# Optimization experiments

Measured on AMD Instinct MI355X. Metric: run time of the kernel, lower is better.

Reference implementation:

```python
import jax, jax.numpy as jnp
import numpy as np

B, K, V_DIM, EMBED, HID, NTOKEN, MAX_LEN = 128, 36, 2048, 1024, 1024, 10000, 20


def _u(key, shape, scale=0.05):
    return jax.random.uniform(key, shape, jnp.float32, -scale, scale)


def setup_inputs() -> dict:
    key = jax.random.key(0)
    ks = jax.random.split(key, 12)
    d1 = HID + V_DIM + EMBED  # word_rnn input size
    d2 = V_DIM + HID          # language_rnn input size
    return dict(
        v=jax.random.normal(ks[0], (B, K, V_DIM), jnp.float32),
        caption=jax.random.normal(ks[1], (B, MAX_LEN, EMBED), jnp.float32),
        cap_len=jnp.sort(jax.random.randint(ks[2], (B,), 2, MAX_LEN + 1))[::-1].astype(jnp.int32),
        Wih1=_u(ks[3], (3 * HID, d1)), Whh1=_u(ks[4], (3 * HID, HID)),
        bih1=jnp.zeros((3 * HID,), jnp.float32), bhh1=jnp.zeros((3 * HID,), jnp.float32),
        Wih2=_u(ks[5], (3 * HID, d2)), Whh2=_u(ks[6], (3 * HID, HID)),
        bih2=jnp.zeros((3 * HID,), jnp.float32), bhh2=jnp.zeros((3 * HID,), jnp.float32),
        Wv=_u(ks[7], (HID, V_DIM)), bv=jnp.zeros((HID,), jnp.float32),
        Wq=_u(ks[8], (HID, HID)), bq=jnp.zeros((HID,), jnp.float32),
        wa=_u(ks[9], (HID,)), ba=jnp.zeros((), jnp.float32),
        W1=_u(ks[10], (HID, HID)), b1=jnp.zeros((HID,), jnp.float32),
        W2=_u(ks[11], (NTOKEN, HID)), b2=jnp.zeros((NTOKEN,), jnp.float32),
    )


def _gru(x, h, Wih, Whh, bih, bhh):
    # PyTorch GRUCell math, gate order (r, z, n)
    gi = x @ Wih.T + bih
    gh = h @ Whh.T + bhh
    ir, iz, inn = jnp.split(gi, 3, axis=-1)
    hr, hz, hn = jnp.split(gh, 3, axis=-1)
    r = jax.nn.sigmoid(ir + hr)
    z = jax.nn.sigmoid(iz + hz)
    n = jnp.tanh(inn + r * hn)
    return (1.0 - z) * n + z * h


def reference(v, caption, cap_len, Wih1, Whh1, bih1, bhh1, Wih2, Whh2, bih2, bhh2,
              Wv, bv, Wq, bq, wa, ba, W1, b1, W2, b2):
    # sort by caption length, descending (as torch forward does)
    order = jnp.argsort(-cap_len)
    v = v[order]
    caption = caption[order]
    cap_len = cap_len[order]
    v_mean = v.mean(1)                                  # [B, V_DIM]
    vproj = jax.nn.relu(v @ Wv.T + bv)                  # [B, K, HID], hoisted out of time loop

    T = MAX_LEN - 1
    dl = cap_len - 1                                    # decode lengths
    mask = (jnp.arange(T)[:, None] < dl[None, :]).astype(v.dtype)   # [T, B]
    prevs = jnp.swapaxes(caption[:, :T, :], 0, 1)       # [T, B, EMBED]

    def step(carry, xs):
        h1, h2 = carry
        prev, m = xs
        h1n = _gru(jnp.concatenate([h2, v_mean, prev], axis=1), h1, Wih1, Whh1, bih1, bhh1)
        hq = h1n @ W1.T + b1                            # h1_fcnet (dropout = identity in eval)
        # 'base' attention: softmax over objects of w^T(relu(Wv v) * relu(Wq q))
        logits = (vproj * jax.nn.relu(hq @ Wq.T + bq)[:, None, :]) @ wa + ba   # [B, K]
        att = jax.nn.softmax(logits, axis=1)
        att_v = jnp.einsum('bk,bkd->bd', att, v)        # attended image feature
        h2n = _gru(jnp.concatenate([att_v, hq], axis=1), h2, Wih2, Whh2, bih2, bhh2)
        word = h2n @ W2.T + b2                          # [B, NTOKEN]
        return (h1n, h2n), (word * m[:, None], att * m[:, None])

    init = (jnp.zeros((B, HID), v.dtype), jnp.zeros((B, HID), v.dtype))
    _, (words, atts) = jax.lax.scan(step, init, (prevs, mask))
    # pad back to max_len timesteps as the torch output buffer does
    predict = jnp.pad(jnp.swapaxes(words, 0, 1), ((0, 0), (0, 1), (0, 0)))   # [B, MAX_LEN, NTOKEN]
    alphas = jnp.pad(jnp.swapaxes(atts, 0, 1), ((0, 0), (0, 1), (0, 0)))     # [B, MAX_LEN, K]
    return predict, alphas
```

## Files before the change

### kernel.cpp

```cpp
#include <hip/hip_runtime.h>
#include <hip/hip_cooperative_groups.h>

namespace cg = cooperative_groups;

typedef unsigned short u16;
typedef __attribute__((ext_vector_type(8))) short bf16x8;
typedef __attribute__((ext_vector_type(4))) float f32x4;

#define NB 128
#define NOBJ 36
#define VDIM 2048
#define EMB 1024
#define HID 1024
#define NTOK 10000
#define MAXLEN 20
#define T_STEPS 19
#define PRED_STRIDE (MAXLEN * NTOK)
#define ALPHA_OFF ((long)NB * MAXLEN * NTOK)
#define HSZ (NB * HID)

struct Args {
  const float *v, *caption;
  const int *cap_len;
  const float *Wih1, *Whh1, *bih1, *bhh1, *Wih2, *Whh2, *bih2, *bhh2;
  const float *Wv, *bv, *Wq, *bq, *wa, *ba, *W1, *b1, *W2, *b2;
  float *out;
  int *order, *dl;
  u16 *Wih1h, *Whh1h, *Wih2h, *Whh2h, *Wvh, *W2h, *vh, *caph, *capl;
  u16 *Wqh, *Wql, *W1T, *Wih2hql, *Wq1u, *Wih2qu;
  u16 *vproj16;
  float *gv1, *gh2s, *h1f, *h2f, *qf, *gcap, *g1a, *g1c, *g2a, *g2b, *gi2h1;
  float *bq1f, *bf2f;
  u16 *h1hi, *h1lo, *h2hi, *h2lo, *avhi, *avlo, *vmhi, *vmlo;
};

__device__ inline float b2f(u16 h) {
  unsigned u = ((unsigned)h) << 16;
  float f;
  __builtin_memcpy(&f, &u, 4);
  return f;
}
__device__ inline u16 f2b_trunc(float x) {
  unsigned u;
  __builtin_memcpy(&u, &x, 4);
  return (u16)(u >> 16);
}
__device__ inline u16 f2b_rne(float x) {
  unsigned u;
  __builtin_memcpy(&u, &x, 4);
  unsigned r = (u + 0x7fffu + ((u >> 16) & 1u)) >> 16;
  return (u16)r;
}
__device__ inline void split_bf16(float x, u16 &hi, u16 &lo) {
  hi = f2b_trunc(x);
  lo = f2b_trunc(x - b2f(hi));
}
__device__ inline bf16x8 ldb8(const u16 *p) {
  uint4 u = *(const uint4 *)p;
  bf16x8 v;
  __builtin_memcpy(&v, &u, 16);
  return v;
}
__device__ inline f32x4 mfma16(bf16x8 a, bf16x8 b, f32x4 c) {
  return __builtin_amdgcn_mfma_f32_16x16x32_bf16(a, b, c, 0, 0, 0);
}
__device__ inline float sigmoidf_(float x) {
  float e = __expf(-fabsf(x));
  float p = 1.f / (1.f + e);
  return x >= 0.f ? p : 1.f - p;
}
__device__ inline float tanhf_(float x) {
  float e = __expf(-2.f * fabsf(x));
  float t = (1.f - e) / (1.f + e);
  return x >= 0.f ? t : -t;
}
__device__ inline float wred_sum(float x) {
#pragma unroll
  for (int off = 32; off > 0; off >>= 1) x += __shfl_xor(x, off, 64);
  return x;
}
__device__ inline float wred_max(float x) {
#pragma unroll
  for (int off = 32; off > 0; off >>= 1) x = fmaxf(x, __shfl_xor(x, off, 64));
  return x;
}

__device__ inline void cvt_hi(const float *src, u16 *dst, long n, long g0,
                              long gs) {
  for (long i = g0 * 4; i < n; i += gs * 4) {
    float4 f = *(const float4 *)(src + i);
    ushort4 o;
    o.x = f2b_rne(f.x);
    o.y = f2b_rne(f.y);
    o.z = f2b_rne(f.z);
    o.w = f2b_rne(f.w);
    *(ushort4 *)(dst + i) = o;
  }
}
__device__ inline void cvt_split(const float *src, u16 *dhi, u16 *dlo, long n,
                                 long g0, long gs) {
  for (long i = g0 * 4; i < n; i += gs * 4) {
    float4 f = *(const float4 *)(src + i);
    ushort4 h, l;
    split_bf16(f.x, h.x, l.x);
    split_bf16(f.y, h.y, l.y);
    split_bf16(f.z, h.z, l.z);
    split_bf16(f.w, h.w, l.w);
    *(ushort4 *)(dhi + i) = h;
    *(ushort4 *)(dlo + i) = l;
  }
}

#define MMK_BODY                                                               \
  {                                                                            \
    const int ko = ks * 32;                                                    \
    bf16x8 va = ldb8(ah + ko);                                                 \
    bf16x8 vl;                                                                 \
    if constexpr (SPLIT) vl = ldb8(al + ko);                                   \
    _Pragma("unroll") for (int i = 0; i < NT; ++i) {                           \
      bf16x8 vb = ldb8(wr + (long)i * wstride + ko);                           \
      acc[i] = mfma16(va, vb, acc[i]);                                         \
      if constexpr (SPLIT) acc[i] = mfma16(vl, vb, acc[i]);                    \
    }                                                                          \
  }

template <int NT, bool SPLIT>
__device__ inline void mmk(f32x4 *acc, const u16 *ah, const u16 *al,
                           const u16 *wr, long wstride, int ksteps) {
  if constexpr (NT == 1) {
#pragma unroll 4
    for (int ks = 0; ks < ksteps; ++ks) MMK_BODY
  } else {
#pragma unroll 2
    for (int ks = 0; ks < ksteps; ++ks) MMK_BODY
  }
}

template <bool SPLIT>
__device__ inline f32x4 tile16(const u16 *ah, const u16 *al, const u16 *wr,
                               int K) {
  f32x4 acc = {0.f, 0.f, 0.f, 0.f};
  mmk<1, SPLIT>(&acc, ah, al, wr, 0, K >> 5);
  return acc;
}

__global__ void __launch_bounds__(512, 4) butd(Args a) {
  cg::grid_group grid = cg::this_grid();
  const int tid = threadIdx.x;
  const int blk = blockIdx.x;
  const int gx = gridDim.x;
  const int lane = tid & 63;
  const int wv = tid >> 6;
  const int m = lane & 15;
  const int quad = lane >> 4;
  __shared__ float sl[64];

  const long gs = (long)gx * 512;
  const long g0 = (long)blk * 512 + tid;

  cvt_hi(a.Wih1, a.Wih1h, 3072L * 4096, g0, gs);
  cvt_hi(a.Whh1, a.Whh1h, 3072L * 1024, g0, gs);
  cvt_hi(a.Wih2, a.Wih2h, 3072L * 3072, g0, gs);
  cvt_hi(a.Whh2, a.Whh2h, 3072L * 1024, g0, gs);
  cvt_hi(a.Wv, a.Wvh, 1024L * 2048, g0, gs);
  cvt_hi(a.W2, a.W2h, (long)NTOK * 1024, g0, gs);
  cvt_hi(a.v, a.vh, (long)NB * NOBJ * VDIM, g0, gs);
  cvt_split(a.caption, a.caph, a.capl, (long)NB * MAXLEN * EMB, g0, gs);
  cvt_split(a.Wq, a.Wqh, a.Wql, 1024L * 1024, g0, gs);
  for (long i = g0; i < 1024L * 1024; i += gs) {
    const int ii = (int)(i >> 10), mm2 = (int)(i & 1023);
    a.W1T[i] = f2b_rne(a.W1[(long)mm2 * 1024 + ii]);
  }
  for (long i = g0 * 4; i < 3072L * 1024; i += gs * 4) {
    const int row = (int)(i >> 10), c = (int)(i & 1023);
    float4 f = *(const float4 *)(a.Wih2 + (long)row * 3072 + 2048 + c);
    ushort4 l;
    l.x = f2b_trunc(f.x - b2f(f2b_rne(f.x)));
    l.y = f2b_trunc(f.y - b2f(f2b_rne(f.y)));
    l.z = f2b_trunc(f.z - b2f(f2b_rne(f.z)));
    l.w = f2b_trunc(f.w - b2f(f2b_rne(f.w)));
    *(ushort4 *)(a.Wih2hql + i) = l;
  }

  if (blk == 0 && tid < NB) {
    int ki = a.cap_len[tid];
    int rank = 0;
    for (int j = 0; j < NB; ++j) {
      int kj = a.cap_len[j];
      rank += (kj > ki) || (kj == ki && j < tid);
    }
    a.order[rank] = tid;
    a.dl[rank] = ki - 1;
  }
  for (long i = g0; i < (long)NB * NTOK; i += gs) {
    long b = i / NTOK, n = i - b * NTOK;
    a.out[b * PRED_STRIDE + (long)(MAXLEN - 1) * NTOK + n] = 0.f;
  }
  for (long i = g0; i < (long)NB * NOBJ; i += gs) {
    long b = i / NOBJ, n = i - b * NOBJ;
    a.out[ALPHA_OFF + b * (MAXLEN * NOBJ) + (MAXLEN - 1) * NOBJ + n] = 0.f;
  }
  for (long i = g0; i < HSZ; i += gs) {
    a.h1f[i] = 0.f;
    a.h2f[i] = 0.f;
    a.h1hi[i] = 0;
    a.h1lo[i] = 0;
    a.h2hi[i] = 0;
    a.h2lo[i] = 0;
  }
  for (long i = g0; i < 128L * 3072; i += gs) a.g1c[i] = 0.f;
  grid.sync();

  for (int b = blk; b < NB; b += gx) {
    const int ob = a.order[b];
    const float *vb = a.v + (long)ob * NOBJ * VDIM;
    for (int d = tid; d < VDIM; d += 512) {
      float s = 0.f;
      for (int k = 0; k < NOBJ; ++k) s += vb[(long)k * VDIM + d];
      s *= (1.f / 36.f);
      u16 hi, lo;
      split_bf16(s, hi, lo);
      a.vmhi[b * VDIM + d] = hi;
      a.vmlo[b * VDIM + d] = lo;
    }
  }
  for (int tt = blk; tt < 576; tt += gx) {
    const int mg = tt % 36, ngr = tt / 36;
    const int row = mg * 128 + wv * 16 + m;
    const int bb = row / NOBJ, ko = row - bb * NOBJ;
    const u16 *ar = a.vh + ((long)a.order[bb] * NOBJ + ko) * VDIM + quad * 8;
    const int c0 = ngr * 64;
    const u16 *wr = a.Wvh + (long)(c0 + m) * VDIM + quad * 8;
    f32x4 acc[4] = {};
    mmk<4, false>(acc, ar, nullptr, wr, 16L * VDIM, VDIM / 32);
#pragma unroll
    for (int i = 0; i < 4; ++i) {
      const int col = c0 + i * 16 + m;
      const float bvv = a.bv[col];
#pragma unroll
      for (int r = 0; r < 4; ++r) {
        const int grow = mg * 128 + wv * 16 + quad * 4 + r;
        a.vproj16[(long)grow * HID + col] = f2b_rne(fmaxf(acc[i][r] + bvv, 0.f));
      }
    }
  }
  for (int o = blk * 8 + wv; o < 4096; o += gx * 8) {
    if (o < 1024) {
      float s = 0.f;
      for (int c = lane; c < 1024; c += 64) s += a.Wq[(long)o * 1024 + c] * a.b1[c];
      s = wred_sum(s);
      if (lane == 0) a.bq1f[o] = s + a.bq[o];
    } else {
      const int oo = o - 1024;
      float s = 0.f;
      for (int c = lane; c < 1024; c += 64)
        s += a.Wih2[(long)oo * 3072 + 2048 + c] * a.b1[c];
      s = wred_sum(s);
      if (lane == 0) a.bf2f[oo] = s;
    }
  }
  grid.sync();

  {
    const int arow = wv * 16 + m;
    for (int task = blk; task < 5888; task += gx) {
      if (task < 192) {
        const int col = task * 16 + m;
        f32x4 acc = tile16<true>(
            a.vmhi + (long)arow * VDIM + quad * 8,
            a.vmlo + (long)arow * VDIM + quad * 8,
            a.Wih1h + (long)col * 4096 + 1024 + quad * 8, VDIM);
        const float bb = a.bih1[col];
#pragma unroll
        for (int r = 0; r < 4; ++r)
          a.gv1[(long)(wv * 16 + quad * 4 + r) * 3072 + col] = acc[r] + bb;
      } else if (task < 3840) {
        const int tt2 = task - 192;
        const int tdx = tt2 / 192, ct = tt2 % 192;
        const int col = ct * 16 + m;
        const long capoff = ((long)a.order[arow] * MAXLEN + tdx) * EMB;
        f32x4 acc = tile16<true>(
            a.caph + capoff + quad * 8, a.capl + capoff + quad * 8,
            a.Wih1h + (long)col * 4096 + 3072 + quad * 8, EMB);
#pragma unroll
        for (int r = 0; r < 4; ++r)
          a.gcap[((long)tdx * NB + wv * 16 + quad * 4 + r) * 3072 + col] =
              acc[r];
      } else if (task < 4352) {
        const int tt2 = task - 3840;
        const int rg = tt2 >> 6, ct = tt2 & 63;
        const int row = rg * 128 + arow, col = ct * 16 + m;
        f32x4 acc = tile16<true>(a.Wqh + (long)row * HID + quad * 8,
                                 a.Wql + (long)row * HID + quad * 8,
                                 a.W1T + (long)col * HID + quad * 8, HID);
#pragma unroll
        for (int r = 0; r < 4; ++r) {
          const int o = rg * 128 + wv * 16 + quad * 4 + r;
          a.Wq1u[(long)o * HID + col] = f2b_rne(acc[r]);
        }
      } else {
        const int tt2 = task - 4352;
        const int rg = tt2 >> 6, ct = tt2 & 63;
        const int row = rg * 128 + arow, col = ct * 16 + m;
        f32x4 acc = tile16<true>(
            a.Wih2h + (long)row * 3072 + 2048 + quad * 8,
            a.Wih2hql + (long)row * HID + quad * 8,
            a.W1T + (long)col * HID + quad * 8, HID);
#pragma unroll
        for (int r = 0; r < 4; ++r) {
          const int o = rg * 128 + wv * 16 + quad * 4 + r;
          a.Wih2qu[(long)o * HID + col] = f2b_rne(acc[r]);
        }
      }
    }
  }
  grid.sync();

  const int arow = wv * 16 + m;

  auto word_tile = [&](int wt, int tf, int pb) {
    const int col = wt * 16 + m;
    f32x4 acc = tile16<true>(
        a.h2hi + (long)pb * HSZ + (long)arow * HID + quad * 8,
        a.h2lo + (long)pb * HSZ + (long)arow * HID + quad * 8,
        a.W2h + (long)col * HID + quad * 8, HID);
    const float bb = a.b2[col];
#pragma unroll
    for (int r = 0; r < 4; ++r) {
      const int grow = wv * 16 + quad * 4 + r;
      const int msk = tf < a.dl[grow];
      a.out[(long)grow * PRED_STRIDE + (long)tf * NTOK + col] =
          msk ? acc[r] + bb : 0.f;
    }
  };

  auto attention = [&](int t, int b, int half) {
    __syncthreads();
    const int ob = a.order[b];
    const float *qrow = a.qf + (long)b * HID;
    for (int k = wv; k < NOBJ; k += 8) {
      const u16 *vp = a.vproj16 + ((long)b * NOBJ + k) * HID;
      float s = 0.f;
      for (int d = lane; d < HID; d += 64) s += b2f(vp[d]) * qrow[d] * a.wa[d];
      s = wred_sum(s);
      if (lane == 0) sl[k] = s + a.ba[0];
    }
    __syncthreads();
    if (wv == 0) {
      float x = (lane < NOBJ) ? sl[lane] : -3.0e38f;
      float mx = wred_max(x);
      float e = (lane < NOBJ) ? __expf(x - mx) : 0.f;
      float den = wred_sum(e);
      float att = e / den;
      if (lane < NOBJ) {
        sl[lane] = att;
        if (half == 0) {
          const int msk = t < a.dl[b];
          a.out[ALPHA_OFF + (long)b * (MAXLEN * NOBJ) + t * NOBJ + lane] =
              msk ? att : 0.f;
        }
      }
    }
    __syncthreads();
    const u16 *vb = a.vh + (long)ob * NOBJ * VDIM + half * 1024;
    for (int d = tid; d < 1024; d += 512) {
      float s = 0.f;
#pragma unroll
      for (int k = 0; k < NOBJ; ++k) s += sl[k] * b2f(vb[(long)k * VDIM + d]);
      u16 hi, lo;
      split_bf16(s, hi, lo);
      a.avhi[(long)b * VDIM + half * 1024 + d] = hi;
      a.avlo[(long)b * VDIM + half * 1024 + d] = lo;
    }
  };

  auto S1 = [&](int t) {
    const int pr = t & 1;
    const u16 *h2h = a.h2hi + (long)pr * HSZ + (long)arow * HID + quad * 8;
    const u16 *h2l = a.h2lo + (long)pr * HSZ + (long)arow * HID + quad * 8;
    for (int task = blk; task < 512; task += gx) {
      if (task < 192) {
        const int col = task * 16 + m;
        f32x4 acc = tile16<true>(h2h, h2l,
                                 a.Wih1h + (long)col * 4096 + quad * 8, HID);
#pragma unroll
        for (int r = 0; r < 4; ++r)
          a.g1a[(long)(wv * 16 + quad * 4 + r) * 3072 + col] = acc[r];
      } else if (task < 384) {
        const int col = (task - 192) * 16 + m;
        f32x4 acc =
            tile16<true>(h2h, h2l, a.Whh2h + (long)col * HID + quad * 8, HID);
        const float bb = a.bhh2[col];
#pragma unroll
        for (int r = 0; r < 4; ++r)
          a.gh2s[(long)(wv * 16 + quad * 4 + r) * 3072 + col] = acc[r] + bb;
      } else if (t > 0) {
        word_tile(task - 384, t - 1, pr);
      }
    }
  };

  auto S2 = [&](int t) {
    const int pr = t & 1, pw_ = pr ^ 1;
    for (long i = g0; i < (long)HSZ; i += gs) {
      const int row = (int)(i >> 10), col = (int)(i & 1023);
      const long o3 = (long)row * 3072 + col;
      const float *gc = a.gcap + ((long)t * NB + row) * 3072 + col;
      float ir = a.g1a[o3] + gc[0] + a.gv1[o3];
      float iz = a.g1a[o3 + 1024] + gc[1024] + a.gv1[o3 + 1024];
      float in_ = a.g1a[o3 + 2048] + gc[2048] + a.gv1[o3 + 2048];
      float hr = a.g1c[o3] + a.bhh1[col];
      float hz = a.g1c[o3 + 1024] + a.bhh1[HID + col];
      float hn = a.g1c[o3 + 2048] + a.bhh1[2 * HID + col];
      float rr = sigmoidf_(ir + hr);
      float zz = sigmoidf_(iz + hz);
      float nn = tanhf_(in_ + rr * hn);
      const long io = (long)pr * HSZ + i, iw = (long)pw_ * HSZ + i;
      float hnew = (1.f - zz) * nn + zz * a.h1f[io];
      a.h1f[iw] = hnew;
      u16 hi, lo;
      split_bf16(hnew, hi, lo);
      a.h1hi[iw] = hi;
      a.h1lo[iw] = lo;
    }
    if (t > 0)
      for (int task = blk; task < 256; task += gx)
        word_tile(128 + task, t - 1, t & 1);
  };

  auto S3 = [&](int t) {
    const int pw_ = (t & 1) ^ 1;
    const u16 *h1h = a.h1hi + (long)pw_ * HSZ + (long)arow * HID + quad * 8;
    const u16 *h1l = a.h1lo + (long)pw_ * HSZ + (long)arow * HID + quad * 8;
    for (int task = blk; task < 497; task += gx) {
      if (task < 64) {
        const int col = task * 16 + m;
        f32x4 acc =
            tile16<true>(h1h, h1l, a.Wq1u + (long)col * HID + quad * 8, HID);
        const float bb = a.bq1f[col];
#pragma unroll
        for (int r = 0; r < 4; ++r)
          a.qf[(long)(wv * 16 + quad * 4 + r) * HID + col] =
              fmaxf(acc[r] + bb, 0.f);
      } else if (task < 256) {
        const int col = (task - 64) * 16 + m;
        f32x4 acc =
            tile16<true>(h1h, h1l, a.Wih2qu + (long)col * HID + quad * 8, HID);
#pragma unroll
        for (int r = 0; r < 4; ++r)
          a.gi2h1[(long)(wv * 16 + quad * 4 + r) * 3072 + col] = acc[r];
      } else if (t > 0) {
        word_tile(384 + (task - 256), t - 1, t & 1);
      }
    }
  };

  auto S4 = [&](int t) {
    const int pw_ = (t & 1) ^ 1;
    for (int task = blk; task < 448; task += gx) {
      if (task < 256) {
        attention(t, task & 127, task >> 7);
      } else if (t + 1 < T_STEPS) {
        const int col = (task - 256) * 16 + m;
        f32x4 acc = tile16<true>(
            a.h1hi + (long)pw_ * HSZ + (long)arow * HID + quad * 8,
            a.h1lo + (long)pw_ * HSZ + (long)arow * HID + quad * 8,
            a.Whh1h + (long)col * HID + quad * 8, HID);
#pragma unroll
        for (int r = 0; r < 4; ++r)
          a.g1c[(long)(wv * 16 + quad * 4 + r) * 3072 + col] = acc[r];
      }
    }
  };

  auto S5 = [&](int t) {
    (void)t;
    for (int task = blk; task < 384; task += gx) {
      const int kh = task / 192, ct = task % 192;
      const int col = ct * 16 + m;
      f32x4 acc = tile16<true>(
          a.avhi + kh * 1024 + (long)arow * VDIM + quad * 8,
          a.avlo + kh * 1024 + (long)arow * VDIM + quad * 8,
          a.Wih2h + (long)col * 3072 + kh * 1024 + quad * 8, HID);
      float *dst = kh ? a.g2b : a.g2a;
#pragma unroll
      for (int r = 0; r < 4; ++r)
        dst[(long)(wv * 16 + quad * 4 + r) * 3072 + col] = acc[r];
    }
  };

  auto S6 = [&](int t) {
    const int pr = t & 1, pw_ = pr ^ 1;
    for (long i = g0; i < (long)HSZ; i += gs) {
      const int row = (int)(i >> 10), col = (int)(i & 1023);
      const long o3 = (long)row * 3072 + col;
      float ir = a.g2a[o3] + a.g2b[o3] + a.gi2h1[o3] + a.bih2[col] + a.bf2f[col];
      float iz = a.g2a[o3 + 1024] + a.g2b[o3 + 1024] + a.gi2h1[o3 + 1024] +
                 a.bih2[HID + col] + a.bf2f[HID + col];
      float in_ = a.g2a[o3 + 2048] + a.g2b[o3 + 2048] + a.gi2h1[o3 + 2048] +
                  a.bih2[2 * HID + col] + a.bf2f[2 * HID + col];
      float hr = a.gh2s[o3], hz = a.gh2s[o3 + 1024], hn = a.gh2s[o3 + 2048];
      float rr = sigmoidf_(ir + hr);
      float zz = sigmoidf_(iz + hz);
      float nn = tanhf_(in_ + rr * hn);
      const long io = (long)pr * HSZ + i, iw = (long)pw_ * HSZ + i;
      float hnew = (1.f - zz) * nn + zz * a.h2f[io];
      a.h2f[iw] = hnew;
      u16 hi, lo;
      split_bf16(hnew, hi, lo);
      a.h2hi[iw] = hi;
      a.h2lo[iw] = lo;
    }
  };

  for (int t = 0; t < T_STEPS; ++t) {
    S1(t);
    grid.sync();
    S2(t);
    grid.sync();
    S3(t);
    grid.sync();
    S4(t);
    grid.sync();
    S5(t);
    grid.sync();
    S6(t);
    grid.sync();
  }
  for (int wt = blk; wt < 625; wt += gx) word_tile(wt, T_STEPS - 1, T_STEPS & 1);
}

extern "C" void kernel_launch(void *const *d_in, const int *in_sizes, int n_in,
                              void *d_out, int out_size, void *d_ws,
                              size_t ws_size, hipStream_t stream) {
  Args a;
  a.v = (const float *)d_in[0];
  a.caption = (const float *)d_in[1];
  a.cap_len = (const int *)d_in[2];
  a.Wih1 = (const float *)d_in[3];
  a.Whh1 = (const float *)d_in[4];
  a.bih1 = (const float *)d_in[5];
  a.bhh1 = (const float *)d_in[6];
  a.Wih2 = (const float *)d_in[7];
  a.Whh2 = (const float *)d_in[8];
  a.bih2 = (const float *)d_in[9];
  a.bhh2 = (const float *)d_in[10];
  a.Wv = (const float *)d_in[11];
  a.bv = (const float *)d_in[12];
  a.Wq = (const float *)d_in[13];
  a.bq = (const float *)d_in[14];
  a.wa = (const float *)d_in[15];
  a.ba = (const float *)d_in[16];
  a.W1 = (const float *)d_in[17];
  a.b1 = (const float *)d_in[18];
  a.W2 = (const float *)d_in[19];
  a.b2 = (const float *)d_in[20];
  a.out = (float *)d_out;

  char *w = (char *)d_ws;
  size_t off = 0;
  auto take = [&](size_t bytes) -> void * {
    void *p = w + off;
    off += (bytes + 255) & ~(size_t)255;
    return p;
  };
  a.order = (int *)take(NB * 4);
  a.dl = (int *)take(NB * 4);
  a.Wih1h = (u16 *)take(3072UL * 4096 * 2);
  a.Whh1h = (u16 *)take(3072UL * 1024 * 2);
  a.Wih2h = (u16 *)take(3072UL * 3072 * 2);
  a.Whh2h = (u16 *)take(3072UL * 1024 * 2);
  a.Wvh = (u16 *)take(1024UL * 2048 * 2);
  a.W2h = (u16 *)take((size_t)NTOK * 1024 * 2);
  a.vh = (u16 *)take((size_t)NB * NOBJ * VDIM * 2);
  a.caph = (u16 *)take((size_t)NB * MAXLEN * EMB * 2);
  a.capl = (u16 *)take((size_t)NB * MAXLEN * EMB * 2);
  a.Wqh = (u16 *)take(1024UL * 1024 * 2);
  a.Wql = (u16 *)take(1024UL * 1024 * 2);
  a.W1T = (u16 *)take(1024UL * 1024 * 2);
  a.Wih2hql = (u16 *)take(3072UL * 1024 * 2);
  a.Wq1u = (u16 *)take(1024UL * 1024 * 2);
  a.Wih2qu = (u16 *)take(3072UL * 1024 * 2);
  a.vproj16 = (u16 *)take((size_t)NB * NOBJ * HID * 2);
  a.gv1 = (float *)take((size_t)NB * 3072 * 4);
  a.gh2s = (float *)take((size_t)NB * 3072 * 4);
  a.h1f = (float *)take((size_t)2 * HSZ * 4);
  a.h2f = (float *)take((size_t)2 * HSZ * 4);
  a.qf = (float *)take((size_t)HSZ * 4);
  a.gcap = (float *)take((size_t)T_STEPS * NB * 3072 * 4);
  a.g1a = (float *)take((size_t)NB * 3072 * 4);
  a.g1c = (float *)take((size_t)NB * 3072 * 4);
  a.g2a = (float *)take((size_t)NB * 3072 * 4);
  a.g2b = (float *)take((size_t)NB * 3072 * 4);
  a.gi2h1 = (float *)take((size_t)NB * 3072 * 4);
  a.bq1f = (float *)take(1024UL * 4);
  a.bf2f = (float *)take(3072UL * 4);
  a.h1hi = (u16 *)take((size_t)2 * HSZ * 2);
  a.h1lo = (u16 *)take((size_t)2 * HSZ * 2);
  a.h2hi = (u16 *)take((size_t)2 * HSZ * 2);
  a.h2lo = (u16 *)take((size_t)2 * HSZ * 2);
  a.avhi = (u16 *)take((size_t)NB * VDIM * 2);
  a.avlo = (u16 *)take((size_t)NB * VDIM * 2);
  a.vmhi = (u16 *)take((size_t)NB * VDIM * 2);
  a.vmlo = (u16 *)take((size_t)NB * VDIM * 2);

  static int gridBlocks = 0;
  if (gridBlocks == 0) {
    int occ = 0;
    if (hipOccupancyMaxActiveBlocksPerMultiprocessor(&occ, (const void *)butd,
                                                     512, 0) != hipSuccess ||
        occ < 1)
      occ = 1;
    gridBlocks = (occ >= 2) ? 512 : 256;
  }

  void *kargs[] = {(void *)&a};
  hipLaunchCooperativeKernel((const void *)butd, dim3(gridBlocks), dim3(512),
                             kargs, 0, stream);
}
```

Baseline: 8.730 ms.

## Replace grid.sync with hierarchical atomic barrier and merge recurrent stages

Swaps cooperative-groups grid.sync for a custom two-level atomic barrier: eight group counters feed one global generation flag. It also folds the query projection into the per-batch attention block, which removes the qf buffer and one grid-wide stage per step. Word-logit tiles and the Whh1/Wih2 projections are redistributed across the remaining five stages. Smaller changes come with it: nontemporal loads and stores for streaming data, separate hi/lo MFMA accumulators in tile16, vectorised attention reductions, and reversed block mapping for the GRU elementwise stages. The trade-off is that each block recomputes a 1024x1024 matvec in scalar code inside attention, and the barrier assumes the block count is a multiple of eight.

```diff
diff --git a/kernel.cpp b/kernel.cpp
--- a/kernel.cpp
+++ b/kernel.cpp
@@ -25,11 +25,12 @@
   const float *Wih1, *Whh1, *bih1, *bhh1, *Wih2, *Whh2, *bih2, *bhh2;
   const float *Wv, *bv, *Wq, *bq, *wa, *ba, *W1, *b1, *W2, *b2;
   float *out;
+  unsigned *bar;
   int *order, *dl;
   u16 *Wih1h, *Whh1h, *Wih2h, *Whh2h, *Wvh, *W2h, *vh, *caph, *capl;
   u16 *Wqh, *Wql, *W1T, *Wih2hql, *Wq1u, *Wih2qu;
   u16 *vproj16;
-  float *gv1, *gh2s, *h1f, *h2f, *qf, *gcap, *g1a, *g1c, *g2a, *g2b, *gi2h1;
+  float *gv1, *gh2s, *h1f, *h2f, *gcap, *g1a, *g1c, *g2a, *g2b, *gi2h1;
   float *bq1f, *bf2f;
   u16 *h1hi, *h1lo, *h2hi, *h2lo, *avhi, *avlo, *vmhi, *vmlo;
 };
@@ -84,28 +85,55 @@
   for (int off = 32; off > 0; off >>= 1) x = fmaxf(x, __shfl_xor(x, off, 64));
   return x;
 }
+__device__ inline void ntstf(float *p, float v) {
+  __builtin_nontemporal_store(v, p);
+}
+__device__ inline f32x4 ntld4(const float *p) {
+  return __builtin_nontemporal_load((const f32x4 *)p);
+}
+
+__device__ inline void gbar(unsigned *bar, int blk, int gx, unsigned gen) {
+  __syncthreads();
+  if (threadIdx.x == 0) {
+    const int g = blk & 7;
+    const unsigned gsz = (unsigned)(gx >> 3);
+    unsigned prev = __hip_atomic_fetch_add(&bar[g * 64], 1u, __ATOMIC_ACQ_REL,
+                                           __HIP_MEMORY_SCOPE_AGENT);
+    if (prev == gen * gsz + gsz - 1) {
+      unsigned p2 = __hip_atomic_fetch_add(&bar[8 * 64], 1u, __ATOMIC_ACQ_REL,
+                                           __HIP_MEMORY_SCOPE_AGENT);
+      if (p2 == gen * 8 + 7)
+        __hip_atomic_store(&bar[9 * 64], gen + 1, __ATOMIC_RELEASE,
+                           __HIP_MEMORY_SCOPE_AGENT);
+    }
+    while (__hip_atomic_load(&bar[9 * 64], __ATOMIC_ACQUIRE,
+                             __HIP_MEMORY_SCOPE_AGENT) <= gen)
+      __builtin_amdgcn_s_sleep(8);
+  }
+  __syncthreads();
+}
 
 __device__ inline void cvt_hi(const float *src, u16 *dst, long n, long g0,
                               long gs) {
   for (long i = g0 * 4; i < n; i += gs * 4) {
-    float4 f = *(const float4 *)(src + i);
+    f32x4 f = ntld4(src + i);
     ushort4 o;
-    o.x = f2b_rne(f.x);
-    o.y = f2b_rne(f.y);
-    o.z = f2b_rne(f.z);
-    o.w = f2b_rne(f.w);
+    o.x = f2b_rne(f[0]);
+    o.y = f2b_rne(f[1]);
+    o.z = f2b_rne(f[2]);
+    o.w = f2b_rne(f[3]);
     *(ushort4 *)(dst + i) = o;
   }
 }
 __device__ inline void cvt_split(const float *src, u16 *dhi, u16 *dlo, long n,
                                  long g0, long gs) {
   for (long i = g0 * 4; i < n; i += gs * 4) {
-    float4 f = *(const float4 *)(src + i);
+    f32x4 f = ntld4(src + i);
     ushort4 h, l;
-    split_bf16(f.x, h.x, l.x);
-    split_bf16(f.y, h.y, l.y);
-    split_bf16(f.z, h.z, l.z);
-    split_bf16(f.w, h.w, l.w);
+    split_bf16(f[0], h.x, l.x);
+    split_bf16(f[1], h.y, l.y);
+    split_bf16(f[2], h.z, l.z);
+    split_bf16(f[3], h.w, l.w);
     *(ushort4 *)(dhi + i) = h;
     *(ushort4 *)(dlo + i) = l;
   }
@@ -127,21 +155,28 @@
 template <int NT, bool SPLIT>
 __device__ inline void mmk(f32x4 *acc, const u16 *ah, const u16 *al,
                            const u16 *wr, long wstride, int ksteps) {
-  if constexpr (NT == 1) {
-#pragma unroll 4
-    for (int ks = 0; ks < ksteps; ++ks) MMK_BODY
-  } else {
 #pragma unroll 2
-    for (int ks = 0; ks < ksteps; ++ks) MMK_BODY
-  }
+  for (int ks = 0; ks < ksteps; ++ks) MMK_BODY
 }
 
 template <bool SPLIT>
 __device__ inline f32x4 tile16(const u16 *ah, const u16 *al, const u16 *wr,
                                int K) {
-  f32x4 acc = {0.f, 0.f, 0.f, 0.f};
-  mmk<1, SPLIT>(&acc, ah, al, wr, 0, K >> 5);
-  return acc;
+  f32x4 acch = {0.f, 0.f, 0.f, 0.f};
+  f32x4 accl = {0.f, 0.f, 0.f, 0.f};
+  const int ksteps = K >> 5;
+#pragma unroll 4
+  for (int ks = 0; ks < ksteps; ++ks) {
+    const int ko = ks * 32;
+    bf16x8 vb = ldb8(wr + ko);
+    acch = mfma16(ldb8(ah + ko), vb, acch);
+    if constexpr (SPLIT) accl = mfma16(ldb8(al + ko), vb, accl);
+  }
+  if constexpr (SPLIT) {
+#pragma unroll
+    for (int r = 0; r < 4; ++r) acch[r] += accl[r];
+  }
+  return acch;
 }
 
 __global__ void __launch_bounds__(512, 4) butd(Args a) {
@@ -154,9 +189,15 @@
   const int m = lane & 15;
   const int quad = lane >> 4;
   __shared__ float sl[64];
+  __shared__ float h1s[HID];
+  __shared__ float qa[HID];
 
   const long gs = (long)gx * 512;
   const long g0 = (long)blk * 512 + tid;
+  unsigned bgen = 0;
+  auto GB = [&]() { gbar(a.bar, blk, gx, bgen++); };
+
+  if (blk == 0 && tid < 16) a.bar[tid * 64] = 0;
 
   cvt_hi(a.Wih1, a.Wih1h, 3072L * 4096, g0, gs);
   cvt_hi(a.Whh1, a.Whh1h, 3072L * 1024, g0, gs);
@@ -173,12 +214,12 @@
   }
   for (long i = g0 * 4; i < 3072L * 1024; i += gs * 4) {
     const int row = (int)(i >> 10), c = (int)(i & 1023);
-    float4 f = *(const float4 *)(a.Wih2 + (long)row * 3072 + 2048 + c);
+    f32x4 f = ntld4(a.Wih2 + (long)row * 3072 + 2048 + c);
     ushort4 l;
-    l.x = f2b_trunc(f.x - b2f(f2b_rne(f.x)));
-    l.y = f2b_trunc(f.y - b2f(f2b_rne(f.y)));
-    l.z = f2b_trunc(f.z - b2f(f2b_rne(f.z)));
-    l.w = f2b_trunc(f.w - b2f(f2b_rne(f.w)));
+    l.x = f2b_trunc(f[0] - b2f(f2b_rne(f[0])));
+    l.y = f2b_trunc(f[1] - b2f(f2b_rne(f[1])));
+    l.z = f2b_trunc(f[2] - b2f(f2b_rne(f[2])));
+    l.w = f2b_trunc(f[3] - b2f(f2b_rne(f[3])));
     *(ushort4 *)(a.Wih2hql + i) = l;
   }
 
@@ -194,11 +235,12 @@
   }
   for (long i = g0; i < (long)NB * NTOK; i += gs) {
     long b = i / NTOK, n = i - b * NTOK;
-    a.out[b * PRED_STRIDE + (long)(MAXLEN - 1) * NTOK + n] = 0.f;
+    ntstf(&a.out[b * PRED_STRIDE + (long)(MAXLEN - 1) * NTOK + n], 0.f);
   }
   for (long i = g0; i < (long)NB * NOBJ; i += gs) {
     long b = i / NOBJ, n = i - b * NOBJ;
-    a.out[ALPHA_OFF + b * (MAXLEN * NOBJ) + (MAXLEN - 1) * NOBJ + n] = 0.f;
+    ntstf(&a.out[ALPHA_OFF + b * (MAXLEN * NOBJ) + (MAXLEN - 1) * NOBJ + n],
+          0.f);
   }
   for (long i = g0; i < HSZ; i += gs) {
     a.h1f[i] = 0.f;
@@ -259,16 +301,16 @@
       if (lane == 0) a.bf2f[oo] = s;
     }
   }
-  grid.sync();
+  GB();
 
   {
-    const int arow = wv * 16 + m;
+    const int arow0 = wv * 16 + m;
     for (int task = blk; task < 5888; task += gx) {
       if (task < 192) {
         const int col = task * 16 + m;
         f32x4 acc = tile16<true>(
-            a.vmhi + (long)arow * VDIM + quad * 8,
-            a.vmlo + (long)arow * VDIM + quad * 8,
+            a.vmhi + (long)arow0 * VDIM + quad * 8,
+            a.vmlo + (long)arow0 * VDIM + quad * 8,
             a.Wih1h + (long)col * 4096 + 1024 + quad * 8, VDIM);
         const float bb = a.bih1[col];
 #pragma unroll
@@ -278,7 +320,7 @@
         const int tt2 = task - 192;
         const int tdx = tt2 / 192, ct = tt2 % 192;
         const int col = ct * 16 + m;
-        const long capoff = ((long)a.order[arow] * MAXLEN + tdx) * EMB;
+        const long capoff = ((long)a.order[arow0] * MAXLEN + tdx) * EMB;
         f32x4 acc = tile16<true>(
             a.caph + capoff + quad * 8, a.capl + capoff + quad * 8,
             a.Wih1h + (long)col * 4096 + 3072 + quad * 8, EMB);
@@ -289,7 +331,7 @@
       } else if (task < 4352) {
         const int tt2 = task - 3840;
         const int rg = tt2 >> 6, ct = tt2 & 63;
-        const int row = rg * 128 + arow, col = ct * 16 + m;
+        const int row = rg * 128 + arow0, col = ct * 16 + m;
         f32x4 acc = tile16<true>(a.Wqh + (long)row * HID + quad * 8,
                                  a.Wql + (long)row * HID + quad * 8,
                                  a.W1T + (long)col * HID + quad * 8, HID);
@@ -301,7 +343,7 @@
       } else {
         const int tt2 = task - 4352;
         const int rg = tt2 >> 6, ct = tt2 & 63;
-        const int row = rg * 128 + arow, col = ct * 16 + m;
+        const int row = rg * 128 + arow0, col = ct * 16 + m;
         f32x4 acc = tile16<true>(
             a.Wih2h + (long)row * 3072 + 2048 + quad * 8,
             a.Wih2hql + (long)row * HID + quad * 8,
@@ -314,7 +356,7 @@
       }
     }
   }
-  grid.sync();
+  GB();
 
   const int arow = wv * 16 + m;
 
@@ -329,19 +371,38 @@
     for (int r = 0; r < 4; ++r) {
       const int grow = wv * 16 + quad * 4 + r;
       const int msk = tf < a.dl[grow];
-      a.out[(long)grow * PRED_STRIDE + (long)tf * NTOK + col] =
-          msk ? acc[r] + bb : 0.f;
-    }
-  };
-
-  auto attention = [&](int t, int b, int half) {
+      ntstf(&a.out[(long)grow * PRED_STRIDE + (long)tf * NTOK + col],
+            msk ? acc[r] + bb : 0.f);
+    }
+  };
+
+  auto attention = [&](int t, int b) {
     __syncthreads();
+    const int pw_ = (t & 1) ^ 1;
     const int ob = a.order[b];
-    const float *qrow = a.qf + (long)b * HID;
+    const float *h1row = a.h1f + (long)pw_ * HSZ + (long)b * HID;
+    for (int d = tid; d < HID; d += 512) h1s[d] = h1row[d];
+    __syncthreads();
+    for (int o = tid; o < HID; o += 512) {
+      const u16 *wr = a.Wq1u + (long)o * HID;
+      float s = 0.f;
+#pragma unroll 4
+      for (int k = 0; k < HID; k += 8) {
+        bf16x8 w8 = ldb8(wr + k);
+#pragma unroll
+        for (int j = 0; j < 8; ++j) s += b2f((u16)w8[j]) * h1s[k + j];
+      }
+      qa[o] = fmaxf(s + a.bq1f[o], 0.f) * a.wa[o];
+    }
+    __syncthreads();
     for (int k = wv; k < NOBJ; k += 8) {
       const u16 *vp = a.vproj16 + ((long)b * NOBJ + k) * HID;
       float s = 0.f;
-      for (int d = lane; d < HID; d += 64) s += b2f(vp[d]) * qrow[d] * a.wa[d];
+      for (int d0 = lane * 8; d0 < HID; d0 += 512) {
+        bf16x8 vv = ldb8(vp + d0);
+#pragma unroll
+        for (int j = 0; j < 8; ++j) s += b2f((u16)vv[j]) * qa[d0 + j];
+      }
       s = wred_sum(s);
       if (lane == 0) sl[k] = s + a.ba[0];
     }
@@ -354,23 +415,35 @@
       float att = e / den;
       if (lane < NOBJ) {
         sl[lane] = att;
-        if (half == 0) {
-          const int msk = t < a.dl[b];
-          a.out[ALPHA_OFF + (long)b * (MAXLEN * NOBJ) + t * NOBJ + lane] =
-              msk ? att : 0.f;
-        }
+        const int msk = t < a.dl[b];
+        ntstf(&a.out[ALPHA_OFF + (long)b * (MAXLEN * NOBJ) + t * NOBJ + lane],
+              msk ? att : 0.f);
       }
     }
     __syncthreads();
-    const u16 *vb = a.vh + (long)ob * NOBJ * VDIM + half * 1024;
-    for (int d = tid; d < 1024; d += 512) {
-      float s = 0.f;
-#pragma unroll
-      for (int k = 0; k < NOBJ; ++k) s += sl[k] * b2f(vb[(long)k * VDIM + d]);
-      u16 hi, lo;
-      split_bf16(s, hi, lo);
-      a.avhi[(long)b * VDIM + half * 1024 + d] = hi;
-      a.avlo[(long)b * VDIM + half * 1024 + d] = lo;
+    if (tid < 256) {
+      const int d0 = tid * 8;
+      const u16 *vb = a.vh + (long)ob * NOBJ * VDIM;
+      float s[8] = {};
+      for (int k = 0; k < NOBJ; ++k) {
+        bf16x8 vv = ldb8(vb + (long)k * VDIM + d0);
+        const float w = sl[k];
+#pragma unroll
+        for (int j = 0; j < 8; ++j) s[j] += w * b2f((u16)vv[j]);
+      }
+      ushort4 h0, h1v, l0, l1v;
+      split_bf16(s[0], h0.x, l0.x);
+      split_bf16(s[1], h0.y, l0.y);
+      split_bf16(s[2], h0.z, l0.z);
+      split_bf16(s[3], h0.w, l0.w);
+      split_bf16(s[4], h1v.x, l1v.x);
+      split_bf16(s[5], h1v.y, l1v.y);
+      split_bf16(s[6], h1v.z, l1v.z);
+      split_bf16(s[7], h1v.w, l1v.w);
+      *(ushort4 *)(a.avhi + (long)b * VDIM + d0) = h0;
+      *(ushort4 *)(a.avhi + (long)b * VDIM + d0 + 4) = h1v;
+      *(ushort4 *)(a.avlo + (long)b * VDIM + d0) = l0;
+      *(ushort4 *)(a.avlo + (long)b * VDIM + d0 + 4) = l1v;
     }
   };
 
@@ -402,7 +475,9 @@
 
   auto S2 = [&](int t) {
     const int pr = t & 1, pw_ = pr ^ 1;
-    for (long i = g0; i < (long)HSZ; i += gs) {
+    const long h0 = (long)(gx - 1 - blk) * 512 + tid;
+    if (h0 < (long)HSZ) {
+      const long i = h0;
       const int row = (int)(i >> 10), col = (int)(i & 1023);
       const long o3 = (long)row * 3072 + col;
       const float *gc = a.gcap + ((long)t * NB + row) * 3072 + col;
@@ -424,74 +499,64 @@
       a.h1lo[iw] = lo;
     }
     if (t > 0)
-      for (int task = blk; task < 256; task += gx)
-        word_tile(128 + task, t - 1, t & 1);
-  };
-
-  auto S3 = [&](int t) {
+      for (int task = blk; task < 192; task += gx)
+        word_tile(128 + task, t - 1, pr);
+  };
+
+  auto S34 = [&](int t) {
+    const int pr = t & 1, pw_ = pr ^ 1;
+    for (int task = blk; task < 500; task += gx) {
+      if (task < 180) {
+        if (t > 0) word_tile(320 + task, t - 1, pr);
+      } else if (task < 372) {
+        if (t + 1 < T_STEPS) {
+          const int col = (task - 180) * 16 + m;
+          f32x4 acc = tile16<true>(
+              a.h1hi + (long)pw_ * HSZ + (long)arow * HID + quad * 8,
+              a.h1lo + (long)pw_ * HSZ + (long)arow * HID + quad * 8,
+              a.Whh1h + (long)col * HID + quad * 8, HID);
+#pragma unroll
+          for (int r = 0; r < 4; ++r)
+            a.g1c[(long)(wv * 16 + quad * 4 + r) * 3072 + col] = acc[r];
+        }
+      } else {
+        attention(t, task - 372);
+      }
+    }
+  };
+
+  auto S5 = [&](int t) {
     const int pw_ = (t & 1) ^ 1;
-    const u16 *h1h = a.h1hi + (long)pw_ * HSZ + (long)arow * HID + quad * 8;
-    const u16 *h1l = a.h1lo + (long)pw_ * HSZ + (long)arow * HID + quad * 8;
-    for (int task = blk; task < 497; task += gx) {
-      if (task < 64) {
-        const int col = task * 16 + m;
-        f32x4 acc =
-            tile16<true>(h1h, h1l, a.Wq1u + (long)col * HID + quad * 8, HID);
-        const float bb = a.bq1f[col];
+    for (int task = blk; task < 576; task += gx) {
+      if (task < 384) {
+        const int kh = task / 192, ct = task % 192;
+        const int col = ct * 16 + m;
+        f32x4 acc = tile16<true>(
+            a.avhi + kh * 1024 + (long)arow * VDIM + quad * 8,
+            a.avlo + kh * 1024 + (long)arow * VDIM + quad * 8,
+            a.Wih2h + (long)col * 3072 + kh * 1024 + quad * 8, HID);
+        float *dst = kh ? a.g2b : a.g2a;
 #pragma unroll
         for (int r = 0; r < 4; ++r)
-          a.qf[(long)(wv * 16 + quad * 4 + r) * HID + col] =
-              fmaxf(acc[r] + bb, 0.f);
-      } else if (task < 256) {
-        const int col = (task - 64) * 16 + m;
-        f32x4 acc =
-            tile16<true>(h1h, h1l, a.Wih2qu + (long)col * HID + quad * 8, HID);
-#pragma unroll
-        for (int r = 0; r < 4; ++r)
-          a.gi2h1[(long)(wv * 16 + quad * 4 + r) * 3072 + col] = acc[r];
-      } else if (t > 0) {
-        word_tile(384 + (task - 256), t - 1, t & 1);
-      }
-    }
-  };
-
-  auto S4 = [&](int t) {
-    const int pw_ = (t & 1) ^ 1;
-    for (int task = blk; task < 448; task += gx) {
-      if (task < 256) {
-        attention(t, task & 127, task >> 7);
-      } else if (t + 1 < T_STEPS) {
-        const int col = (task - 256) * 16 + m;
+          dst[(long)(wv * 16 + quad * 4 + r) * 3072 + col] = acc[r];
+      } else {
+        const int col = (task - 384) * 16 + m;
         f32x4 acc = tile16<true>(
             a.h1hi + (long)pw_ * HSZ + (long)arow * HID + quad * 8,
             a.h1lo + (long)pw_ * HSZ + (long)arow * HID + quad * 8,
-            a.Whh1h + (long)col * HID + quad * 8, HID);
+            a.Wih2qu + (long)col * HID + quad * 8, HID);
 #pragma unroll
         for (int r = 0; r < 4; ++r)
-          a.g1c[(long)(wv * 16 + quad * 4 + r) * 3072 + col] = acc[r];
-      }
-    }
-  };
-
-  auto S5 = [&](int t) {
-    (void)t;
-    for (int task = blk; task < 384; task += gx) {
-      const int kh = task / 192, ct = task % 192;
-      const int col = ct * 16 + m;
-      f32x4 acc = tile16<true>(
-          a.avhi + kh * 1024 + (long)arow * VDIM + quad * 8,
-          a.avlo + kh * 1024 + (long)arow * VDIM + quad * 8,
-          a.Wih2h + (long)col * 3072 + kh * 1024 + quad * 8, HID);
-      float *dst = kh ? a.g2b : a.g2a;
-#pragma unroll
-      for (int r = 0; r < 4; ++r)
-        dst[(long)(wv * 16 + quad * 4 + r) * 3072 + col] = acc[r];
+          a.gi2h1[(long)(wv * 16 + quad * 4 + r) * 3072 + col] = acc[r];
+      }
     }
   };
 
   auto S6 = [&](int t) {
     const int pr = t & 1, pw_ = pr ^ 1;
-    for (long i = g0; i < (long)HSZ; i += gs) {
+    const long h0 = (long)(gx - 1 - blk) * 512 + tid;
+    if (h0 < (long)HSZ) {
+      const long i = h0;
       const int row = (int)(i >> 10), col = (int)(i & 1023);
       const long o3 = (long)row * 3072 + col;
       float ir = a.g2a[o3] + a.g2b[o3] + a.gi2h1[o3] + a.bih2[col] + a.bf2f[col];
@@ -511,21 +576,22 @@
       a.h2hi[iw] = hi;
       a.h2lo[iw] = lo;
     }
+    if (t > 0)
+      for (int task = blk; task < 125; task += gx)
+        word_tile(500 + task, t - 1, pr);
   };
 
   for (int t = 0; t < T_STEPS; ++t) {
     S1(t);
-    grid.sync();
+    GB();
     S2(t);
-    grid.sync();
-    S3(t);
-    grid.sync();
-    S4(t);
-    grid.sync();
+    GB();
+    S34(t);
+    GB();
     S5(t);
-    grid.sync();
+    GB();
     S6(t);
-    grid.sync();
+    GB();
   }
   for (int wt = blk; wt < 625; wt += gx) word_tile(wt, T_STEPS - 1, T_STEPS & 1);
 }
@@ -564,6 +630,7 @@
     off += (bytes + 255) & ~(size_t)255;
     return p;
   };
+  a.bar = (unsigned *)take(4096);
   a.order = (int *)take(NB * 4);
   a.dl = (int *)take(NB * 4);
   a.Wih1h = (u16 *)take(3072UL * 4096 * 2);
@@ -586,7 +653,6 @@
   a.gh2s = (float *)take((size_t)NB * 3072 * 4);
   a.h1f = (float *)take((size_t)2 * HSZ * 4);
   a.h2f = (float *)take((size_t)2 * HSZ * 4);
-  a.qf = (float *)take((size_t)HSZ * 4);
   a.gcap = (float *)take((size_t)T_STEPS * NB * 3072 * 4);
   a.g1a = (float *)take((size_t)NB * 3072 * 4);
   a.g1c = (float *)take((size_t)NB * 3072 * 4);
```

After: 24.99 ms. 2.86x slower.
